# Kernel tuning notes

Hardware: AMD Instinct MI355X
Metric: run time of the kernel (lower is better)

Reference implementation:

```python
import jax, jax.numpy as jnp
import numpy as np

B, Q, K, F = 4, 512, 512, 32
DV = 32          # vnode feature dim
H = 64           # proj_vs output dim
FM = 2 * F + DV + 2 + 1 + 1 + 1  # = 101, pairwise concat feature dim
H1, H2 = 256, 64 # proj_scores hidden widths
MAX_DIST = 1e30  # default max_dist = inf


def _dense_init(key, fan_in, fan_out):
    kw, kb = jax.random.split(key)
    W = jax.random.normal(kw, (fan_in, fan_out), jnp.float32) / np.sqrt(fan_in)
    b = jnp.zeros((fan_out,), jnp.float32)
    return W, b


def setup_inputs() -> dict:
    key = jax.random.key(0)
    ks_ = jax.random.split(key, 13)
    qs = jax.random.normal(ks_[0], (B, Q, F), jnp.float32)
    ks = jax.random.normal(ks_[1], (B, K, F), jnp.float32)
    vs = jax.random.normal(ks_[2], (B, K, F), jnp.float32)
    vnode = jax.random.normal(ks_[3], (B, 1, DV), jnp.float32)
    qs_s = jax.random.normal(ks_[4], (B, Q, 2), jnp.float32)
    ks_s = jax.random.normal(ks_[5], (B, K, 2), jnp.float32)
    qs_t = jnp.ones((B, Q, 1), jnp.float32)                     # queries at t=1
    ks_t = jax.random.uniform(ks_[6], (B, K, 1), jnp.float32)   # keys in [0,1)
    valid_lens = jax.random.randint(ks_[7], (B,), 1, K + 1).astype(jnp.int32)
    Ws1, bs1 = _dense_init(ks_[8], FM, H1)
    Ws2, bs2 = _dense_init(ks_[9], H1, H2)
    Ws3, bs3 = _dense_init(ks_[10], H2, 1)
    Wv, bv = _dense_init(ks_[11], F, H)
    return {"qs": qs, "ks": ks, "vs": vs, "vnode": vnode,
            "qs_s": qs_s, "ks_s": ks_s, "qs_t": qs_t, "ks_t": ks_t,
            "Ws1": Ws1, "bs1": bs1, "Ws2": Ws2, "bs2": bs2,
            "Ws3": Ws3, "bs3": bs3, "Wv": Wv, "bv": bv,
            "valid_lens": valid_lens}


def reference(qs, ks, vs, vnode, qs_s, ks_s, qs_t, ks_t,
              Ws1, bs1, Ws2, bs2, Ws3, bs3, Wv, bv, valid_lens):
    Bq, Qq, Ff = qs.shape
    Kk = ks.shape[1]
    # pairwise broadcast of q/k/vnode features -> [B, Q, K, *]
    qe = jnp.broadcast_to(qs[:, :, None, :], (Bq, Qq, Kk, Ff))
    ke = jnp.broadcast_to(ks[:, None, :, :], (Bq, Qq, Kk, Ff))
    vn = jnp.broadcast_to(vnode[:, :, None, :], (Bq, Qq, Kk, vnode.shape[-1]))
    # spatial pairwise features
    s_diff = qs_s[:, :, None, :] - ks_s[:, None, :, :]          # [B,Q,K,2]
    s_dist = jnp.linalg.norm(s_diff, axis=-1, keepdims=True)    # [B,Q,K,1]
    s_dist_sq = jnp.square(s_dist)
    # temporal pairwise feature
    t_diff = qs_t[:, :, None, :] - ks_t[:, None, :, :]          # [B,Q,K,1]
    m = jnp.concatenate([qe, ke, vn, s_diff, s_dist, s_dist_sq, t_diff], axis=-1)
    # mask: valid key length, spatial radius, causal time
    key_mask = jnp.arange(Kk)[None, :] < valid_lens[:, None]    # [B,K]
    mask = key_mask[:, None, :]                                  # [B,1,K] -> broadcast [B,Q,K]
    mask = jnp.logical_and(mask, s_dist[..., 0] <= MAX_DIST)
    mask = jnp.logical_and(mask, t_diff[..., 0] >= 0)
    # proj_scores MLP: Dense-gelu-Dense-gelu-Dense
    h = jax.nn.gelu(m @ Ws1 + bs1)
    h = jax.nn.gelu(h @ Ws2 + bs2)
    scores = (h @ Ws3 + bs3)[..., 0]                             # [B,Q,K]
    scores = jnp.where(mask, scores, -jnp.inf)
    attn = jax.nn.softmax(scores, axis=-1)
    vproj = vs @ Wv + bv                                         # [B,K,H]
    ctx = jnp.einsum('bqk,bkh->bqh', attn, vproj)
    return ctx, attn
```

## Files before the change

kernel.cpp:

```cpp
#include <hip/hip_runtime.h>

#define B_ 4
#define Q_ 512
#define K_ 512
#define F_ 32
#define H1_ 256
#define H2_ 64
#define HV_ 64

typedef unsigned short u16;
typedef unsigned int u32;

typedef float f32x4 __attribute__((ext_vector_type(4)));
typedef short short8 __attribute__((ext_vector_type(8)));
typedef __bf16 bfv8 __attribute__((ext_vector_type(8)));
union FRG { short8 s; bfv8 h; u32 u[4]; };

#define OFF_QS   0
#define OFF_KS   65536
#define OFF_VS   131072
#define OFF_VN   196608
#define OFF_QSS  196736
#define OFF_KSS  200832
#define OFF_QST  204928
#define OFF_KST  206976
#define OFF_W1   209024
#define OFF_B1   234880
#define OFF_W2   235136
#define OFF_B2   243328
#define OFF_W3   243392
#define OFF_B3   243456
#define OFF_WV   243460
#define OFF_BV   245508
#define OFF_VL   245572
#define OFF_AQ   262144
#define OFF_AK   786432
#define OFF_VP   1310720

__device__ __forceinline__ float bf2f(u16 u) {
    union { u32 u; float f; } c; c.u = ((u32)u) << 16; return c.f;
}
__device__ __forceinline__ u16 f2bf(float f) {
    union { float f; u32 u; } c; c.f = f;
    u32 u = c.u;
    return (u16)((u + 0x7FFFu + ((u >> 16) & 1u)) >> 16);
}
__device__ __forceinline__ float gelu_t(float x) {
    const float Kb = 2.3022082f;
    const float Kc = 0.10294324f;
    float y = x * __builtin_fmaf(Kc, x * x, Kb);
    float e = __builtin_amdgcn_exp2f(y);
    return x - x * __builtin_amdgcn_rcpf(e + 1.0f);
}

__global__ __launch_bounds__(256) void convert_kernel(
    const void* s0, const void* s1, const void* s2, const void* s3,
    const void* s4, const void* s5, const void* s6, const void* s7,
    const void* s8, const void* s9, const void* s10, const void* s11,
    const void* s12, const void* s13, const void* s14, const void* s15,
    const void* s16, float* wsf)
{
    int blk = blockIdx.x, t = threadIdx.x;
    int bf16m = (((const u32*)s6)[0] != 0x3F800000u);

    if (blk == 963) {
        if (t < 4) {
            const int* vi = (const int*)s16;
            int is64 = (vi[1] == 0);
            ((int*)(wsf + OFF_VL))[t] = vi[is64 ? 2 * t : t];
        }
        return;
    }
    if (blk >= 919 && blk < 951) {
        int idx = (blk - 919) * 256 + t;
        int r  = idx & 3;
        int l  = (idx >> 2) & 63;
        int n  = (idx >> 8) & 3;
        int ks = idx >> 10;
        int k0  = ks * 32 + (l >> 4) * 8 + 2 * r;
        int col = n * 16 + (l & 15);
        u16 lo, hi;
        if (bf16m) {
            lo = ((const u16*)s10)[k0 * H2_ + col];
            hi = ((const u16*)s10)[(k0 + 1) * H2_ + col];
        } else {
            lo = f2bf(((const float*)s10)[k0 * H2_ + col]);
            hi = f2bf(((const float*)s10)[(k0 + 1) * H2_ + col]);
        }
        ((u32*)(wsf + OFF_W2))[idx] = (u32)lo | ((u32)hi << 16);
        return;
    }
    const void* src; int n, dst, b0;
    if      (blk < 256) { src = s0;  n = 65536; dst = OFF_QS;  b0 = 0;   }
    else if (blk < 512) { src = s1;  n = 65536; dst = OFF_KS;  b0 = 256; }
    else if (blk < 768) { src = s2;  n = 65536; dst = OFF_VS;  b0 = 512; }
    else if (blk < 769) { src = s3;  n = 128;   dst = OFF_VN;  b0 = 768; }
    else if (blk < 785) { src = s4;  n = 4096;  dst = OFF_QSS; b0 = 769; }
    else if (blk < 801) { src = s5;  n = 4096;  dst = OFF_KSS; b0 = 785; }
    else if (blk < 809) { src = s6;  n = 2048;  dst = OFF_QST; b0 = 801; }
    else if (blk < 817) { src = s7;  n = 2048;  dst = OFF_KST; b0 = 809; }
    else if (blk < 918) { src = s8;  n = 25856; dst = OFF_W1;  b0 = 817; }
    else if (blk < 919) { src = s9;  n = 256;   dst = OFF_B1;  b0 = 918; }
    else if (blk < 952) { src = s11; n = 64;    dst = OFF_B2;  b0 = 951; }
    else if (blk < 953) { src = s12; n = 64;    dst = OFF_W3;  b0 = 952; }
    else if (blk < 954) { src = s13; n = 1;     dst = OFF_B3;  b0 = 953; }
    else if (blk < 962) { src = s14; n = 2048;  dst = OFF_WV;  b0 = 954; }
    else                { src = s15; n = 64;    dst = OFF_BV;  b0 = 962; }
    int idx = (blk - b0) * 256 + t;
    if (idx < n)
        (wsf + dst)[idx] = bf16m ? bf2f(((const u16*)src)[idx]) : ((const float*)src)[idx];
}

__global__ __launch_bounds__(256) void prep_kernel(
    const float* __restrict__ qs, const float* __restrict__ ks, const float* __restrict__ vs,
    const float* __restrict__ vnode, const float* __restrict__ qs_s, const float* __restrict__ ks_s,
    const float* __restrict__ qs_t, const float* __restrict__ ks_t,
    const float* __restrict__ W1, const float* __restrict__ b1,
    const float* __restrict__ Wv, const float* __restrict__ bv,
    float* __restrict__ Aq, float* __restrict__ Ak, float* __restrict__ vproj)
{
    int blk = blockIdx.x;
    int t = threadIdx.x;
    if (blk < 2048) {
        int b = blk >> 9, q = blk & 511, d = t;
        float acc = b1[d];
        const float* qrow = qs + (b * Q_ + q) * F_;
        #pragma unroll
        for (int f = 0; f < F_; ++f)
            acc = __builtin_fmaf(qrow[f], W1[f * H1_ + d], acc);
        const float* vn = vnode + b * 32;
        #pragma unroll
        for (int f = 0; f < 32; ++f)
            acc = __builtin_fmaf(vn[f], W1[(64 + f) * H1_ + d], acc);
        float q0 = qs_s[(b * Q_ + q) * 2 + 0];
        float q1 = qs_s[(b * Q_ + q) * 2 + 1];
        float qt = qs_t[b * Q_ + q];
        acc = __builtin_fmaf(q0, W1[96 * H1_ + d], acc);
        acc = __builtin_fmaf(q1, W1[97 * H1_ + d], acc);
        acc = __builtin_fmaf(qt, W1[100 * H1_ + d], acc);
        Aq[blk * H1_ + d] = acc;
    } else if (blk < 4096) {
        int rk = blk - 2048;
        int b = rk >> 9, k = rk & 511, d = t;
        float acc = 0.f;
        const float* krow = ks + (b * K_ + k) * F_;
        #pragma unroll
        for (int f = 0; f < F_; ++f)
            acc = __builtin_fmaf(krow[f], W1[(32 + f) * H1_ + d], acc);
        float k0 = ks_s[(b * K_ + k) * 2 + 0];
        float k1 = ks_s[(b * K_ + k) * 2 + 1];
        float kt = ks_t[b * K_ + k];
        acc = __builtin_fmaf(-k0, W1[96 * H1_ + d], acc);
        acc = __builtin_fmaf(-k1, W1[97 * H1_ + d], acc);
        acc = __builtin_fmaf(-kt, W1[100 * H1_ + d], acc);
        Ak[(b * K_ + k) * H1_ + d] = acc;
    } else {
        int idx = (blk - 4096) * 256 + t;
        int h = idx & 63;
        int k = (idx >> 6) & 511;
        int b = idx >> 15;
        float acc = bv[h];
        const float* vrow = vs + (b * K_ + k) * F_;
        #pragma unroll
        for (int f = 0; f < F_; ++f)
            acc = __builtin_fmaf(vrow[f], Wv[f * HV_ + h], acc);
        vproj[idx] = acc;
    }
}

__global__ __launch_bounds__(256, 4) void fused_kernel(
    const float* __restrict__ qs_s, const float* __restrict__ ks_s,
    const float* __restrict__ qs_t, const float* __restrict__ ks_t,
    const float* __restrict__ W1, const u32* __restrict__ W2F,
    const float* __restrict__ b2, const float* __restrict__ W3, const float* __restrict__ b3,
    const int* __restrict__ vl, const float* __restrict__ Aq, const float* __restrict__ Ak,
    const float* __restrict__ vproj, const void* __restrict__ qs_t_src, void* __restrict__ d_out)
{
    __shared__ __align__(16) float sAq[H1_], sw98[H1_], sw99[H1_];
    __shared__ float sScore[K_];
    __shared__ float sE[K_];
    __shared__ float sRed[16];
    __shared__ float sPart[4][HV_];

    int q = blockIdx.x, b = blockIdx.y, t = threadIdx.x;
    int lane = t & 63, w = t >> 6;
    int VL = vl[b];
    int nT = (VL + 15) >> 4;

    sAq[t]  = Aq[(b * Q_ + q) * H1_ + t];
    sw98[t] = W1[98 * H1_ + t];
    sw99[t] = W1[99 * H1_ + t];
    __syncthreads();

    float q0x = qs_s[(b * Q_ + q) * 2 + 0];
    float q1x = qs_s[(b * Q_ + q) * 2 + 1];
    float qtx = qs_t[b * Q_ + q];

    float b2c[4], w3c[4];
    #pragma unroll
    for (int n = 0; n < 4; ++n) {
        int col = n * 16 + (lane & 15);
        b2c[n] = b2[col];
        w3c[n] = W3[col];
    }
    float b3v = b3[0];
    const float* Ak_b = Ak + (size_t)b * K_ * H1_;
    int lgrp = (lane >> 4) * 8;

    for (int tile = w; tile < nT; tile += 4) {
        int row = tile * 16 + (lane & 15);
        float c0 = ks_s[(b * K_ + row) * 2 + 0];
        float c1 = ks_s[(b * K_ + row) * 2 + 1];
        float ktv = ks_t[b * K_ + row];
        float d0 = q0x - c0, d1 = q1x - c1;
        float dsq  = __builtin_fmaf(d0, d0, d1 * d1);
        float dist = sqrtf(dsq);
        float okf = (row < VL && (qtx - ktv) >= 0.f && dist <= 1e30f) ? 1.f : 0.f;

        f32x4 acc[4];
        #pragma unroll
        for (int n = 0; n < 4; ++n) acc[n] = (f32x4){0.f, 0.f, 0.f, 0.f};

        const float* akrow = Ak_b + row * H1_;
        #pragma unroll 4
        for (int ks = 0; ks < 8; ++ks) {
            int dbase = ks * 32 + lgrp;
            f32x4 aqa  = *(const f32x4*)&sAq[dbase];
            f32x4 aqb  = *(const f32x4*)&sAq[dbase + 4];
            f32x4 w98a = *(const f32x4*)&sw98[dbase];
            f32x4 w98b = *(const f32x4*)&sw98[dbase + 4];
            f32x4 w99a = *(const f32x4*)&sw99[dbase];
            f32x4 w99b = *(const f32x4*)&sw99[dbase + 4];
            f32x4 ak0 = *(const f32x4*)(akrow + dbase);
            f32x4 ak1 = *(const f32x4*)(akrow + dbase + 4);
            short8 bf[4];
            #pragma unroll
            for (int n = 0; n < 4; ++n)
                bf[n] = *(const short8*)&W2F[((ks * 4 + n) * 64 + lane) * 4];
            FRG fa;
            #pragma unroll
            for (int j = 0; j < 4; ++j) {
                float pre = ak0[j] + __builtin_fmaf(dist, w98a[j],
                           __builtin_fmaf(dsq, w99a[j], aqa[j]));
                fa.h[j] = (__bf16)gelu_t(pre);
            }
            #pragma unroll
            for (int j = 0; j < 4; ++j) {
                float pre = ak1[j] + __builtin_fmaf(dist, w98b[j],
                           __builtin_fmaf(dsq, w99b[j], aqb[j]));
                fa.h[4 + j] = (__bf16)gelu_t(pre);
            }
            #pragma unroll
            for (int n = 0; n < 4; ++n)
                acc[n] = __builtin_amdgcn_mfma_f32_16x16x32_bf16(fa.s, bf[n], acc[n], 0, 0, 0);
        }

        float s0 = 0.f, s1 = 0.f, s2 = 0.f, s3 = 0.f;
        #pragma unroll
        for (int n = 0; n < 4; ++n) {
            f32x4 a = acc[n];
            s0 = __builtin_fmaf(gelu_t(a.x + b2c[n]), w3c[n], s0);
            s1 = __builtin_fmaf(gelu_t(a.y + b2c[n]), w3c[n], s1);
            s2 = __builtin_fmaf(gelu_t(a.z + b2c[n]), w3c[n], s2);
            s3 = __builtin_fmaf(gelu_t(a.w + b2c[n]), w3c[n], s3);
        }
        #pragma unroll
        for (int off = 1; off < 16; off <<= 1) {
            s0 += __shfl_xor(s0, off);
            s1 += __shfl_xor(s1, off);
            s2 += __shfl_xor(s2, off);
            s3 += __shfl_xor(s3, off);
        }
        int g = lane >> 4;
        float ok0 = __shfl(okf, g * 4 + 0);
        float ok1 = __shfl(okf, g * 4 + 1);
        float ok2 = __shfl(okf, g * 4 + 2);
        float ok3 = __shfl(okf, g * 4 + 3);
        if ((lane & 15) == 0) {
            int r0 = tile * 16 + g * 4;
            const float NEG = -__builtin_inff();
            sScore[r0 + 0] = (ok0 != 0.f) ? s0 + b3v : NEG;
            sScore[r0 + 1] = (ok1 != 0.f) ? s1 + b3v : NEG;
            sScore[r0 + 2] = (ok2 != 0.f) ? s2 + b3v : NEG;
            sScore[r0 + 3] = (ok3 != 0.f) ? s3 + b3v : NEG;
        }
    }
    __syncthreads();

    const float NEG = -__builtin_inff();
    float v0 = (t       < VL) ? sScore[t]       : NEG;
    float v1 = (t + 256 < VL) ? sScore[t + 256] : NEG;
    float m = fmaxf(v0, v1);
    #pragma unroll
    for (int off = 32; off > 0; off >>= 1) m = fmaxf(m, __shfl_down(m, off));
    if (lane == 0) sRed[w] = m;
    __syncthreads();
    if (t == 0) sRed[8] = fmaxf(fmaxf(sRed[0], sRed[1]), fmaxf(sRed[2], sRed[3]));
    __syncthreads();
    float mx = sRed[8];

    const float L2E = 1.4426950408889634f;
    int fin = (mx > -1e37f);
    float e0 = (fin && v0 > -1e37f) ? __builtin_amdgcn_exp2f((v0 - mx) * L2E) : 0.f;
    float e1 = (fin && v1 > -1e37f) ? __builtin_amdgcn_exp2f((v1 - mx) * L2E) : 0.f;
    sE[t] = e0; sE[t + 256] = e1;
    float s = e0 + e1;
    #pragma unroll
    for (int off = 32; off > 0; off >>= 1) s += __shfl_down(s, off);
    if (lane == 0) sRed[w] = s;
    __syncthreads();
    if (t == 0) {
        float ss = sRed[0] + sRed[1] + sRed[2] + sRed[3];
        sRed[8] = (ss > 0.f) ? 1.f / ss : 0.f;
    }
    __syncthreads();
    float rinv = sRed[8];

    int bf16m = (((const u32*)qs_t_src)[0] != 0x3F800000u);
    int oattn = B_ * Q_ * HV_ + (b * Q_ + q) * K_;
    if (bf16m) {
        ((u16*)d_out)[oattn + t]       = f2bf(e0 * rinv);
        ((u16*)d_out)[oattn + t + 256] = f2bf(e1 * rinv);
    } else {
        ((float*)d_out)[oattn + t]       = e0 * rinv;
        ((float*)d_out)[oattn + t + 256] = e1 * rinv;
    }

    int h = t & 63, ksp = t >> 6;
    const float* vp = vproj + b * K_ * HV_ + h;
    float acc2 = 0.f;
    int kbeg = ksp * 128;
    for (int kk = kbeg; kk < kbeg + 128; ++kk)
        acc2 = __builtin_fmaf(sE[kk], vp[kk * HV_], acc2);
    sPart[ksp][h] = acc2;
    __syncthreads();
    if (t < HV_) {
        float c = (sPart[0][t] + sPart[1][t] + sPart[2][t] + sPart[3][t]) * rinv;
        int octx = (b * Q_ + q) * HV_ + t;
        if (bf16m) ((u16*)d_out)[octx] = f2bf(c);
        else       ((float*)d_out)[octx] = c;
    }
}

extern "C" void kernel_launch(void* const* d_in, const int* in_sizes, int n_in,
                              void* d_out, int out_size, void* d_ws, size_t ws_size,
                              hipStream_t stream) {
    float* wsf = (float*)d_ws;

    convert_kernel<<<dim3(964), dim3(256), 0, stream>>>(
        d_in[0], d_in[1], d_in[2], d_in[3], d_in[4], d_in[5], d_in[6], d_in[7],
        d_in[8], d_in[9], d_in[10], d_in[11], d_in[12], d_in[13], d_in[14], d_in[15],
        d_in[16], wsf);

    prep_kernel<<<dim3(4608), dim3(256), 0, stream>>>(
        wsf + OFF_QS, wsf + OFF_KS, wsf + OFF_VS, wsf + OFF_VN,
        wsf + OFF_QSS, wsf + OFF_KSS, wsf + OFF_QST, wsf + OFF_KST,
        wsf + OFF_W1, wsf + OFF_B1, wsf + OFF_WV, wsf + OFF_BV,
        wsf + OFF_AQ, wsf + OFF_AK, wsf + OFF_VP);

    fused_kernel<<<dim3(Q_, B_), dim3(256), 0, stream>>>(
        wsf + OFF_QSS, wsf + OFF_KSS, wsf + OFF_QST, wsf + OFF_KST,
        wsf + OFF_W1, (const u32*)(wsf + OFF_W2), wsf + OFF_B2, wsf + OFF_W3, wsf + OFF_B3,
        (const int*)(wsf + OFF_VL), wsf + OFF_AQ, wsf + OFF_AK, wsf + OFF_VP,
        d_in[6], d_out);
}
```

Baseline: 103.1 us.

## Process two queries per block to reuse key rows and W2 fragments

Each block now handles two adjacent queries instead of one, so the Ak row loads, W1 row 98/99 loads, W2 bf16 fragments and vproj loads are shared between two query computations, with two independent MFMA accumulator sets. The grid is halved. This cuts global and LDS traffic per query and gives more independent MFMAs to interleave. In exchange it raises register pressure, which may hurt occupancy under the 256x4 launch bounds, and halves the number of blocks.

```diff
diff --git a/kernel.cpp b/kernel.cpp
--- a/kernel.cpp
+++ b/kernel.cpp
@@ -176,25 +176,31 @@
     const int* __restrict__ vl, const float* __restrict__ Aq, const float* __restrict__ Ak,
     const float* __restrict__ vproj, const void* __restrict__ qs_t_src, void* __restrict__ d_out)
 {
-    __shared__ __align__(16) float sAq[H1_], sw98[H1_], sw99[H1_];
-    __shared__ float sScore[K_];
-    __shared__ float sE[K_];
-    __shared__ float sRed[16];
-    __shared__ float sPart[4][HV_];
-
-    int q = blockIdx.x, b = blockIdx.y, t = threadIdx.x;
+    __shared__ __align__(16) float sAq[2][H1_];
+    __shared__ __align__(16) float sw98[H1_], sw99[H1_];
+    __shared__ float sScore[2][K_];
+    __shared__ float sE[2][K_];
+    __shared__ float sRed[2][12];
+    __shared__ float sPart[2][4][HV_];
+
+    int q0 = blockIdx.x * 2, b = blockIdx.y, t = threadIdx.x;
     int lane = t & 63, w = t >> 6;
     int VL = vl[b];
     int nT = (VL + 15) >> 4;
 
-    sAq[t]  = Aq[(b * Q_ + q) * H1_ + t];
+    sAq[0][t] = Aq[(b * Q_ + q0) * H1_ + t];
+    sAq[1][t] = Aq[(b * Q_ + q0 + 1) * H1_ + t];
     sw98[t] = W1[98 * H1_ + t];
     sw99[t] = W1[99 * H1_ + t];
     __syncthreads();
 
-    float q0x = qs_s[(b * Q_ + q) * 2 + 0];
-    float q1x = qs_s[(b * Q_ + q) * 2 + 1];
-    float qtx = qs_t[b * Q_ + q];
+    float qx0[2], qx1[2], qtv[2];
+    #pragma unroll
+    for (int qq = 0; qq < 2; ++qq) {
+        qx0[qq] = qs_s[(b * Q_ + q0 + qq) * 2 + 0];
+        qx1[qq] = qs_s[(b * Q_ + q0 + qq) * 2 + 1];
+        qtv[qq] = qs_t[b * Q_ + q0 + qq];
+    }
 
     float b2c[4], w3c[4];
     #pragma unroll
@@ -212,21 +218,25 @@
         float c0 = ks_s[(b * K_ + row) * 2 + 0];
         float c1 = ks_s[(b * K_ + row) * 2 + 1];
         float ktv = ks_t[b * K_ + row];
-        float d0 = q0x - c0, d1 = q1x - c1;
-        float dsq  = __builtin_fmaf(d0, d0, d1 * d1);
-        float dist = sqrtf(dsq);
-        float okf = (row < VL && (qtx - ktv) >= 0.f && dist <= 1e30f) ? 1.f : 0.f;
-
-        f32x4 acc[4];
-        #pragma unroll
-        for (int n = 0; n < 4; ++n) acc[n] = (f32x4){0.f, 0.f, 0.f, 0.f};
+        float dsq[2], dist[2], okf[2];
+        #pragma unroll
+        for (int qq = 0; qq < 2; ++qq) {
+            float d0 = qx0[qq] - c0, d1 = qx1[qq] - c1;
+            dsq[qq]  = __builtin_fmaf(d0, d0, d1 * d1);
+            dist[qq] = sqrtf(dsq[qq]);
+            okf[qq] = (row < VL && (qtv[qq] - ktv) >= 0.f && dist[qq] <= 1e30f) ? 1.f : 0.f;
+        }
+
+        f32x4 acc[2][4];
+        #pragma unroll
+        for (int qq = 0; qq < 2; ++qq)
+            #pragma unroll
+            for (int n = 0; n < 4; ++n) acc[qq][n] = (f32x4){0.f, 0.f, 0.f, 0.f};
 
         const float* akrow = Ak_b + row * H1_;
-        #pragma unroll 4
+        #pragma unroll 2
         for (int ks = 0; ks < 8; ++ks) {
             int dbase = ks * 32 + lgrp;
-            f32x4 aqa  = *(const f32x4*)&sAq[dbase];
-            f32x4 aqb  = *(const f32x4*)&sAq[dbase + 4];
             f32x4 w98a = *(const f32x4*)&sw98[dbase];
             f32x4 w98b = *(const f32x4*)&sw98[dbase + 4];
             f32x4 w99a = *(const f32x4*)&sw99[dbase];
@@ -237,106 +247,143 @@
             #pragma unroll
             for (int n = 0; n < 4; ++n)
                 bf[n] = *(const short8*)&W2F[((ks * 4 + n) * 64 + lane) * 4];
-            FRG fa;
-            #pragma unroll
-            for (int j = 0; j < 4; ++j) {
-                float pre = ak0[j] + __builtin_fmaf(dist, w98a[j],
-                           __builtin_fmaf(dsq, w99a[j], aqa[j]));
-                fa.h[j] = (__bf16)gelu_t(pre);
+            FRG fa[2];
+            #pragma unroll
+            for (int qq = 0; qq < 2; ++qq) {
+                f32x4 aqa = *(const f32x4*)&sAq[qq][dbase];
+                f32x4 aqb = *(const f32x4*)&sAq[qq][dbase + 4];
+                #pragma unroll
+                for (int j = 0; j < 4; ++j) {
+                    float pre = ak0[j] + __builtin_fmaf(dist[qq], w98a[j],
+                               __builtin_fmaf(dsq[qq], w99a[j], aqa[j]));
+                    fa[qq].h[j] = (__bf16)gelu_t(pre);
+                }
+                #pragma unroll
+                for (int j = 0; j < 4; ++j) {
+                    float pre = ak1[j] + __builtin_fmaf(dist[qq], w98b[j],
+                               __builtin_fmaf(dsq[qq], w99b[j], aqb[j]));
+                    fa[qq].h[4 + j] = (__bf16)gelu_t(pre);
+                }
             }
             #pragma unroll
-            for (int j = 0; j < 4; ++j) {
-                float pre = ak1[j] + __builtin_fmaf(dist, w98b[j],
-                           __builtin_fmaf(dsq, w99b[j], aqb[j]));
-                fa.h[4 + j] = (__bf16)gelu_t(pre);
+            for (int n = 0; n < 4; ++n) {
+                acc[0][n] = __builtin_amdgcn_mfma_f32_16x16x32_bf16(fa[0].s, bf[n], acc[0][n], 0, 0, 0);
+                acc[1][n] = __builtin_amdgcn_mfma_f32_16x16x32_bf16(fa[1].s, bf[n], acc[1][n], 0, 0, 0);
             }
-            #pragma unroll
-            for (int n = 0; n < 4; ++n)
-                acc[n] = __builtin_amdgcn_mfma_f32_16x16x32_bf16(fa.s, bf[n], acc[n], 0, 0, 0);
-        }
-
-        float s0 = 0.f, s1 = 0.f, s2 = 0.f, s3 = 0.f;
-        #pragma unroll
-        for (int n = 0; n < 4; ++n) {
-            f32x4 a = acc[n];
-            s0 = __builtin_fmaf(gelu_t(a.x + b2c[n]), w3c[n], s0);
-            s1 = __builtin_fmaf(gelu_t(a.y + b2c[n]), w3c[n], s1);
-            s2 = __builtin_fmaf(gelu_t(a.z + b2c[n]), w3c[n], s2);
-            s3 = __builtin_fmaf(gelu_t(a.w + b2c[n]), w3c[n], s3);
-        }
-        #pragma unroll
-        for (int off = 1; off < 16; off <<= 1) {
-            s0 += __shfl_xor(s0, off);
-            s1 += __shfl_xor(s1, off);
-            s2 += __shfl_xor(s2, off);
-            s3 += __shfl_xor(s3, off);
-        }
-        int g = lane >> 4;
-        float ok0 = __shfl(okf, g * 4 + 0);
-        float ok1 = __shfl(okf, g * 4 + 1);
-        float ok2 = __shfl(okf, g * 4 + 2);
-        float ok3 = __shfl(okf, g * 4 + 3);
-        if ((lane & 15) == 0) {
-            int r0 = tile * 16 + g * 4;
-            const float NEG = -__builtin_inff();
-            sScore[r0 + 0] = (ok0 != 0.f) ? s0 + b3v : NEG;
-            sScore[r0 + 1] = (ok1 != 0.f) ? s1 + b3v : NEG;
-            sScore[r0 + 2] = (ok2 != 0.f) ? s2 + b3v : NEG;
-            sScore[r0 + 3] = (ok3 != 0.f) ? s3 + b3v : NEG;
+        }
+
+        #pragma unroll
+        for (int qq = 0; qq < 2; ++qq) {
+            float s0 = 0.f, s1 = 0.f, s2 = 0.f, s3 = 0.f;
+            #pragma unroll
+            for (int n = 0; n < 4; ++n) {
+                f32x4 a = acc[qq][n];
+                s0 = __builtin_fmaf(gelu_t(a.x + b2c[n]), w3c[n], s0);
+                s1 = __builtin_fmaf(gelu_t(a.y + b2c[n]), w3c[n], s1);
+                s2 = __builtin_fmaf(gelu_t(a.z + b2c[n]), w3c[n], s2);
+                s3 = __builtin_fmaf(gelu_t(a.w + b2c[n]), w3c[n], s3);
+            }
+            #pragma unroll
+            for (int off = 1; off < 16; off <<= 1) {
+                s0 += __shfl_xor(s0, off);
+                s1 += __shfl_xor(s1, off);
+                s2 += __shfl_xor(s2, off);
+                s3 += __shfl_xor(s3, off);
+            }
+            int g = lane >> 4;
+            float ok0 = __shfl(okf[qq], g * 4 + 0);
+            float ok1 = __shfl(okf[qq], g * 4 + 1);
+            float ok2 = __shfl(okf[qq], g * 4 + 2);
+            float ok3 = __shfl(okf[qq], g * 4 + 3);
+            if ((lane & 15) == 0) {
+                int r0 = tile * 16 + g * 4;
+                const float NEG = -__builtin_inff();
+                sScore[qq][r0 + 0] = (ok0 != 0.f) ? s0 + b3v : NEG;
+                sScore[qq][r0 + 1] = (ok1 != 0.f) ? s1 + b3v : NEG;
+                sScore[qq][r0 + 2] = (ok2 != 0.f) ? s2 + b3v : NEG;
+                sScore[qq][r0 + 3] = (ok3 != 0.f) ? s3 + b3v : NEG;
+            }
         }
     }
     __syncthreads();
 
     const float NEG = -__builtin_inff();
-    float v0 = (t       < VL) ? sScore[t]       : NEG;
-    float v1 = (t + 256 < VL) ? sScore[t + 256] : NEG;
-    float m = fmaxf(v0, v1);
-    #pragma unroll
-    for (int off = 32; off > 0; off >>= 1) m = fmaxf(m, __shfl_down(m, off));
-    if (lane == 0) sRed[w] = m;
-    __syncthreads();
-    if (t == 0) sRed[8] = fmaxf(fmaxf(sRed[0], sRed[1]), fmaxf(sRed[2], sRed[3]));
-    __syncthreads();
-    float mx = sRed[8];
+    float v0[2], v1[2], mred[2];
+    #pragma unroll
+    for (int qq = 0; qq < 2; ++qq) {
+        v0[qq] = (t       < VL) ? sScore[qq][t]       : NEG;
+        v1[qq] = (t + 256 < VL) ? sScore[qq][t + 256] : NEG;
+        mred[qq] = fmaxf(v0[qq], v1[qq]);
+    }
+    #pragma unroll
+    for (int off = 32; off > 0; off >>= 1) {
+        mred[0] = fmaxf(mred[0], __shfl_down(mred[0], off));
+        mred[1] = fmaxf(mred[1], __shfl_down(mred[1], off));
+    }
+    if (lane == 0) { sRed[0][w] = mred[0]; sRed[1][w] = mred[1]; }
+    __syncthreads();
+    if (t == 0) {
+        sRed[0][8] = fmaxf(fmaxf(sRed[0][0], sRed[0][1]), fmaxf(sRed[0][2], sRed[0][3]));
+        sRed[1][8] = fmaxf(fmaxf(sRed[1][0], sRed[1][1]), fmaxf(sRed[1][2], sRed[1][3]));
+    }
+    __syncthreads();
 
     const float L2E = 1.4426950408889634f;
-    int fin = (mx > -1e37f);
-    float e0 = (fin && v0 > -1e37f) ? __builtin_amdgcn_exp2f((v0 - mx) * L2E) : 0.f;
-    float e1 = (fin && v1 > -1e37f) ? __builtin_amdgcn_exp2f((v1 - mx) * L2E) : 0.f;
-    sE[t] = e0; sE[t + 256] = e1;
-    float s = e0 + e1;
-    #pragma unroll
-    for (int off = 32; off > 0; off >>= 1) s += __shfl_down(s, off);
-    if (lane == 0) sRed[w] = s;
+    float e0[2], e1[2], sum[2];
+    #pragma unroll
+    for (int qq = 0; qq < 2; ++qq) {
+        float mx = sRed[qq][8];
+        int fin = (mx > -1e37f);
+        e0[qq] = (fin && v0[qq] > -1e37f) ? __builtin_amdgcn_exp2f((v0[qq] - mx) * L2E) : 0.f;
+        e1[qq] = (fin && v1[qq] > -1e37f) ? __builtin_amdgcn_exp2f((v1[qq] - mx) * L2E) : 0.f;
+        sE[qq][t] = e0[qq]; sE[qq][t + 256] = e1[qq];
+        sum[qq] = e0[qq] + e1[qq];
+    }
+    #pragma unroll
+    for (int off = 32; off > 0; off >>= 1) {
+        sum[0] += __shfl_down(sum[0], off);
+        sum[1] += __shfl_down(sum[1], off);
+    }
+    if (lane == 0) { sRed[0][w] = sum[0]; sRed[1][w] = sum[1]; }
     __syncthreads();
     if (t == 0) {
-        float ss = sRed[0] + sRed[1] + sRed[2] + sRed[3];
-        sRed[8] = (ss > 0.f) ? 1.f / ss : 0.f;
-    }
-    __syncthreads();
-    float rinv = sRed[8];
+        float s0 = sRed[0][0] + sRed[0][1] + sRed[0][2] + sRed[0][3];
+        float s1 = sRed[1][0] + sRed[1][1] + sRed[1][2] + sRed[1][3];
+        sRed[0][8] = (s0 > 0.f) ? 1.f / s0 : 0.f;
+        sRed[1][8] = (s1 > 0.f) ? 1.f / s1 : 0.f;
+    }
+    __syncthreads();
+    float rinv[2] = { sRed[0][8], sRed[1][8] };
 
     int bf16m = (((const u32*)qs_t_src)[0] != 0x3F800000u);
-    int oattn = B_ * Q_ * HV_ + (b * Q_ + q) * K_;
-    if (bf16m) {
-        ((u16*)d_out)[oattn + t]       = f2bf(e0 * rinv);
-        ((u16*)d_out)[oattn + t + 256] = f2bf(e1 * rinv);
-    } else {
-        ((float*)d_out)[oattn + t]       = e0 * rinv;
-        ((float*)d_out)[oattn + t + 256] = e1 * rinv;
+    #pragma unroll
+    for (int qq = 0; qq < 2; ++qq) {
+        int oattn = B_ * Q_ * HV_ + (b * Q_ + q0 + qq) * K_;
+        if (bf16m) {
+            ((u16*)d_out)[oattn + t]       = f2bf(e0[qq] * rinv[qq]);
+            ((u16*)d_out)[oattn + t + 256] = f2bf(e1[qq] * rinv[qq]);
+        } else {
+            ((float*)d_out)[oattn + t]       = e0[qq] * rinv[qq];
+            ((float*)d_out)[oattn + t + 256] = e1[qq] * rinv[qq];
+        }
     }
 
     int h = t & 63, ksp = t >> 6;
     const float* vp = vproj + b * K_ * HV_ + h;
-    float acc2 = 0.f;
+    float a0 = 0.f, a1 = 0.f;
     int kbeg = ksp * 128;
-    for (int kk = kbeg; kk < kbeg + 128; ++kk)
-        acc2 = __builtin_fmaf(sE[kk], vp[kk * HV_], acc2);
-    sPart[ksp][h] = acc2;
-    __syncthreads();
-    if (t < HV_) {
-        float c = (sPart[0][t] + sPart[1][t] + sPart[2][t] + sPart[3][t]) * rinv;
-        int octx = (b * Q_ + q) * HV_ + t;
+    for (int kk = kbeg; kk < kbeg + 128; ++kk) {
+        float v = vp[kk * HV_];
+        a0 = __builtin_fmaf(sE[0][kk], v, a0);
+        a1 = __builtin_fmaf(sE[1][kk], v, a1);
+    }
+    sPart[0][ksp][h] = a0;
+    sPart[1][ksp][h] = a1;
+    __syncthreads();
+    if (t < 128) {
+        int qq = t >> 6, hh = t & 63;
+        float c = (sPart[qq][0][hh] + sPart[qq][1][hh] + sPart[qq][2][hh] + sPart[qq][3][hh]) * rinv[qq];
+        int octx = (b * Q_ + q0 + qq) * HV_ + hh;
         if (bf16m) ((u16*)d_out)[octx] = f2bf(c);
         else       ((float*)d_out)[octx] = c;
     }
@@ -358,7 +405,7 @@
         wsf + OFF_W1, wsf + OFF_B1, wsf + OFF_WV, wsf + OFF_BV,
         wsf + OFF_AQ, wsf + OFF_AK, wsf + OFF_VP);
 
-    fused_kernel<<<dim3(Q_, B_), dim3(256), 0, stream>>>(
+    fused_kernel<<<dim3(Q_ / 2, B_), dim3(256), 0, stream>>>(
         wsf + OFF_QSS, wsf + OFF_KSS, wsf + OFF_QST, wsf + OFF_KST,
         wsf + OFF_W1, (const u32*)(wsf + OFF_W2), wsf + OFF_B2, wsf + OFF_W3, wsf + OFF_B3,
         (const int*)(wsf + OFF_VL), wsf + OFF_AQ, wsf + OFF_AK, wsf + OFF_VP,
```

Result: faster. 86.68 us (-15.9%).
